# Kernel tuning notes

Measured on AMD Instinct MI355X. Metric: run time of the kernel, lower is better.

The kernel has to match this reference:

```python
import jax, jax.numpy as jnp
import numpy as np

N_NODES = 10000
N_EDGES = 80000
IN_DIM = 768
HID = 256
HEADS = 8
NEG_SLOPE = 0.2


def setup_inputs() -> dict:
    key = jax.random.key(0)
    ks = jax.random.split(key, 12)
    s = 0.02
    x = jax.random.normal(ks[0], (N_NODES, IN_DIM), dtype=jnp.float32)
    edge_index = jax.random.randint(ks[1], (2, N_EDGES), 0, N_NODES, dtype=jnp.int64)
    W1 = jax.random.normal(ks[2], (IN_DIM, HEADS * HID), dtype=jnp.float32) * s
    a_src1 = jax.random.normal(ks[3], (HEADS, HID), dtype=jnp.float32) * s
    a_dst1 = jax.random.normal(ks[4], (HEADS, HID), dtype=jnp.float32) * s
    b1 = jnp.zeros((HEADS * HID,), dtype=jnp.float32)
    W2 = jax.random.normal(ks[5], (HEADS * HID, HEADS * HID), dtype=jnp.float32) * s
    a_src2 = jax.random.normal(ks[6], (HEADS, HID), dtype=jnp.float32) * s
    a_dst2 = jax.random.normal(ks[7], (HEADS, HID), dtype=jnp.float32) * s
    b2 = jnp.zeros((HID,), dtype=jnp.float32)
    # graph_projection: 256 -> 256
    Wp = jax.random.normal(ks[8], (HID, HID), dtype=jnp.float32) * s
    bp = jnp.zeros((HID,), dtype=jnp.float32)
    return dict(x=x, edge_index=edge_index, W1=W1, a_src1=a_src1, a_dst1=a_dst1,
                b1=b1, W2=W2, a_src2=a_src2, a_dst2=a_dst2, b2=b2, Wp=Wp, bp=bp)


def _gat_conv(x, src, dst, W, a_src, a_dst, b, concat):
    """PyG GATConv (eval mode, self-loops already appended to src/dst)."""
    N = x.shape[0]
    H, C = a_src.shape
    h = (x @ W).reshape(N, H, C)                         # [N,H,C] per-head projection
    alpha_s = jnp.sum(h * a_src[None], axis=-1)           # [N,H]
    alpha_d = jnp.sum(h * a_dst[None], axis=-1)           # [N,H]
    e = jax.nn.leaky_relu(alpha_s[src] + alpha_d[dst], NEG_SLOPE)  # [E,H]
    # segment softmax over incoming edges of each dst node
    m = jax.ops.segment_max(e, dst, num_segments=N)       # [N,H]
    m = jnp.where(jnp.isfinite(m), m, 0.0)
    p = jnp.exp(e - m[dst])
    denom = jax.ops.segment_sum(p, dst, num_segments=N)   # [N,H]
    alpha = p / (denom[dst] + 1e-16)                      # [E,H]
    out = jax.ops.segment_sum(alpha[:, :, None] * h[src], dst, num_segments=N)  # [N,H,C]
    if concat:
        return out.reshape(N, H * C) + b
    return out.mean(axis=1) + b


def reference(x, edge_index, W1, a_src1, a_dst1, b1, W2, a_src2, a_dst2, b2, Wp, bp):
    N = x.shape[0]
    loops = jnp.arange(N, dtype=edge_index.dtype)
    src = jnp.concatenate([edge_index[0], loops])
    dst = jnp.concatenate([edge_index[1], loops])
    h = _gat_conv(x, src, dst, W1, a_src1, a_dst1, b1, concat=True)   # [N, 2048]
    h = jax.nn.elu(h)                                                 # dropout: eval/no-op
    h = _gat_conv(h, src, dst, W2, a_src2, a_dst2, b2, concat=False)  # [N, 256]
    h = h @ Wp + bp
    return jax.nn.relu(h)                                             # dropout: eval/no-op
```

## Files before the change

kernel.cpp:

```cpp
#include <hip/hip_runtime.h>
#include <cstdint>
#include <cstddef>

#define IN_DIM  768
#define NNODES  10000
#define MPAD    10240
#define NEDGES  80000
#define E_TOT   90000
#define HEADS   8
#define HID     256
#define HC      2048
#define NEG_SLOPE 0.2f

#define CVT_BLK  ((MPAD * IN_DIM / 4) / 256)
#define CNT_BLK  ((E_TOT + 255) / 256)
#define T1_BLK   ((HC / 32) * (IN_DIM / 32))
#define T2_BLK   ((HC / 32) * (HC / 32))
#define TP_BLK   ((HID / 32) * (HID / 32))
#define PREP_BLK (CVT_BLK + CNT_BLK + T1_BLK + T2_BLK + TP_BLK)

typedef _Float16 __attribute__((ext_vector_type(8))) f16x8;
typedef float    __attribute__((ext_vector_type(4))) f32x4;

__device__ __forceinline__ int edge_src(const int* __restrict__ ei, int e) {
    return (e < NEDGES) ? ei[e] : (e - NEDGES);
}
__device__ __forceinline__ int edge_dst(const int* __restrict__ ei, int e) {
    return (e < NEDGES) ? ei[NEDGES + e] : (e - NEDGES);
}

__device__ __forceinline__ void tcvt_body(
    const float* __restrict__ W, _Float16* __restrict__ T,
    int K, int N, int bx, int by, int t)
{
    __shared__ float tile[32][33];
    int tx = t & 31, ty = t >> 5;
#pragma unroll
    for (int q = 0; q < 4; q++)
        tile[ty + q * 8][tx] = W[(size_t)(by * 32 + ty + q * 8) * N + bx * 32 + tx];
    __syncthreads();
#pragma unroll
    for (int q = 0; q < 4; q++) {
        float v = tile[tx][ty + q * 8];
        T[(size_t)(bx * 32 + ty + q * 8) * K + by * 32 + tx] = (_Float16)v;
    }
}

__global__ __launch_bounds__(256) void prep_kernel(
    const float* __restrict__ x, _Float16* __restrict__ xh,
    const int* __restrict__ ei, int* __restrict__ cnt,
    const float* __restrict__ W1, _Float16* __restrict__ W1t,
    const float* __restrict__ W2, _Float16* __restrict__ W2t,
    const float* __restrict__ Wp, _Float16* __restrict__ Wpt)
{
    int b = blockIdx.x;
    int t = threadIdx.x;
    if (b < CVT_BLK) {
        int i = b * 256 + t;
        size_t e = (size_t)i * 4;
        int r = (int)(e / IN_DIM);
        float4 v = (r < NNODES) ? *(const float4*)(x + e)
                                : make_float4(0.f, 0.f, 0.f, 0.f);
        _Float16 h4[4] = {(_Float16)v.x, (_Float16)v.y, (_Float16)v.z, (_Float16)v.w};
        *(ushort4*)(xh + e) = *(ushort4*)h4;
    } else if (b < CVT_BLK + CNT_BLK) {
        int e = (b - CVT_BLK) * 256 + t;
        if (e < E_TOT) atomicAdd(&cnt[edge_dst(ei, e)], 1);
    } else if (b < CVT_BLK + CNT_BLK + T1_BLK) {
        int idx = b - (CVT_BLK + CNT_BLK);
        tcvt_body(W1, W1t, IN_DIM, HC, idx % (HC / 32), idx / (HC / 32), t);
    } else if (b < CVT_BLK + CNT_BLK + T1_BLK + T2_BLK) {
        int idx = b - (CVT_BLK + CNT_BLK + T1_BLK);
        tcvt_body(W2, W2t, HC, HC, idx % (HC / 32), idx / (HC / 32), t);
    } else {
        int idx = b - (CVT_BLK + CNT_BLK + T1_BLK + T2_BLK);
        tcvt_body(Wp, Wpt, HID, HID, idx % (HID / 32), idx / (HID / 32), t);
    }
}

__global__ void scan_kernel(const int* __restrict__ cnt, int* __restrict__ indptr) {
    __shared__ int sums[1024];
    const int CH = 10;
    int t = threadIdx.x;
    int base = t * CH;
    int s = 0;
#pragma unroll
    for (int i = 0; i < CH; i++) { int idx = base + i; if (idx < NNODES) s += cnt[idx]; }
    sums[t] = s;
    __syncthreads();
    for (int off = 1; off < 1024; off <<= 1) {
        int v = (t >= off) ? sums[t - off] : 0;
        __syncthreads();
        sums[t] += v;
        __syncthreads();
    }
    int run = (t == 0) ? 0 : sums[t - 1];
#pragma unroll
    for (int i = 0; i < CH; i++) {
        int idx = base + i;
        if (idx < NNODES) { indptr[idx] = run; run += cnt[idx]; }
    }
    if (t == 0) indptr[NNODES] = E_TOT;
}

__global__ void scatter_kernel(const int* __restrict__ ei, const int* __restrict__ indptr,
                               int* __restrict__ cur, int* __restrict__ sorted) {
    int e = blockIdx.x * 256 + threadIdx.x;
    if (e < E_TOT) {
        int d = edge_dst(ei, e);
        int pos = atomicAdd(&cur[d], 1);
        sorted[indptr[d] + pos] = e;
    }
}

__global__ __launch_bounds__(512, 2) void gemm8p_kernel(
    const _Float16* __restrict__ A, const _Float16* __restrict__ B,
    _Float16* __restrict__ C, int M, int K, int Nn,
    const float* __restrict__ asrc, const float* __restrict__ adst,
    float* __restrict__ as_out, float* __restrict__ ad_out)
{
    __shared__ __align__(16) _Float16 lds[2][36864];

    const int t = threadIdx.x;
    const int w = t >> 6, lane = t & 63;
    const int fr = lane & 15, q4 = lane >> 4;
    const int wr = w >> 2, wc = w & 3;

    const int nwgx = gridDim.x;
    int wg = blockIdx.y * nwgx + blockIdx.x;
    const int cpx = (nwgx * gridDim.y) >> 3;
    wg = (wg & 7) * cpx + (wg >> 3);
    const int row0 = (wg / nwgx) * 320;
    const int col0 = (wg % nwgx) * 256;

    const int rowt = t >> 3;
    const int scol = ((t & 7) ^ (rowt & 7)) << 3;
    const _Float16* baseA = A + (size_t)(row0 + rowt) * K + scol;
    const _Float16* baseB = B + (size_t)(col0 + rowt) * K + scol;
    const int dstw = w * 512;

    auto stageA = [&](int q, int kel, int bb) {
        __builtin_amdgcn_global_load_lds(
            (const __attribute__((address_space(1))) void*)(baseA + (size_t)q * 64 * K + kel),
            (__attribute__((address_space(3))) void*)&lds[bb][q * 4096 + dstw], 16, 0, 0);
    };
    auto stageB = [&](int q, int kel, int bb) {
        __builtin_amdgcn_global_load_lds(
            (const __attribute__((address_space(1))) void*)(baseB + (size_t)q * 64 * K + kel),
            (__attribute__((address_space(3))) void*)&lds[bb][20480 + q * 4096 + dstw], 16, 0, 0);
    };

    f32x4 acc[2][2][5][2];
#pragma unroll
    for (int qm = 0; qm < 2; qm++)
#pragma unroll
        for (int qn = 0; qn < 2; qn++)
#pragma unroll
            for (int mi = 0; mi < 5; mi++)
#pragma unroll
                for (int ni = 0; ni < 2; ni++)
                    acc[qm][qn][mi][ni] = {0.f, 0.f, 0.f, 0.f};

    f16x8 fa[5][2], fb[2][2][2];

#define LOADA(BB, QM)                                                           \
    {                                                                           \
        _Pragma("unroll")                                                       \
        for (int mi = 0; mi < 5; mi++) {                                        \
            _Pragma("unroll")                                                   \
            for (int ks = 0; ks < 2; ks++) {                                    \
                int lr = wr * 80 + mi * 16 + fr;                                \
                int sl = ((ks << 2) | q4) ^ (fr & 7);                           \
                fa[mi][ks] = *(const f16x8*)&lds[BB][(QM) * 10240 + (lr << 6) + (sl << 3)]; \
            }                                                                   \
        }                                                                       \
    }
#define LOADB(BB, QN)                                                           \
    {                                                                           \
        _Pragma("unroll")                                                       \
        for (int ni = 0; ni < 2; ni++) {                                        \
            _Pragma("unroll")                                                   \
            for (int ks = 0; ks < 2; ks++) {                                    \
                int lr = wc * 32 + ni * 16 + fr;                                \
                int sl = ((ks << 2) | q4) ^ (fr & 7);                           \
                fb[QN][ni][ks] = *(const f16x8*)&lds[BB][20480 + (QN) * 8192 + (lr << 6) + (sl << 3)]; \
            }                                                                   \
        }                                                                       \
    }
#define MFMAQ(QM, QN)                                                           \
    {                                                                           \
        _Pragma("unroll")                                                       \
        for (int ks = 0; ks < 2; ks++) {                                        \
            _Pragma("unroll")                                                   \
            for (int mi = 0; mi < 5; mi++) {                                    \
                _Pragma("unroll")                                               \
                for (int ni = 0; ni < 2; ni++)                                  \
                    acc[QM][QN][mi][ni] = __builtin_amdgcn_mfma_f32_16x16x32_f16(\
                        fa[mi][ks], fb[QN][ni][ks], acc[QM][QN][mi][ni], 0, 0, 0); \
            }                                                                   \
        }                                                                       \
    }
#define LG0 do { asm volatile("s_waitcnt lgkmcnt(0)" ::: "memory");             \
                 __builtin_amdgcn_sched_barrier(0); } while (0)

    stageA(0, 0, 0); stageA(1, 0, 0); stageA(2, 0, 0);
    stageB(0, 0, 0); stageB(1, 0, 0); stageB(2, 0, 0); stageB(3, 0, 0);
    stageA(3, 0, 0); stageA(4, 0, 0);

    const int nT = K >> 6;
    for (int t0 = 0; t0 < nT; ++t0) {
        const int bb = t0 & 1, bn = bb ^ 1, k1 = (t0 + 1) << 6;
        const bool pf = (t0 + 1 < nT);
        asm volatile("s_waitcnt vmcnt(0)" ::: "memory");
        __builtin_amdgcn_s_barrier();

        LOADA(bb, 0); LOADB(bb, 0);
        if (pf) { stageA(0, k1, bn); stageA(1, k1, bn); stageA(2, k1, bn); }
        LG0;
        __builtin_amdgcn_s_setprio(1); MFMAQ(0, 0); __builtin_amdgcn_s_setprio(0);
        __builtin_amdgcn_sched_barrier(0);

        LOADB(bb, 1);
        if (pf) { stageB(0, k1, bn); stageB(1, k1, bn); stageB(2, k1, bn); stageB(3, k1, bn); }
        LG0;
        __builtin_amdgcn_s_setprio(1); MFMAQ(0, 1); __builtin_amdgcn_s_setprio(0);
        __builtin_amdgcn_sched_barrier(0);

        LOADA(bb, 1);
        if (pf) { stageA(3, k1, bn); stageA(4, k1, bn); }
        LG0;
        __builtin_amdgcn_s_setprio(1); MFMAQ(1, 1); MFMAQ(1, 0); __builtin_amdgcn_s_setprio(0);
        __builtin_amdgcn_sched_barrier(0);
    }
#undef LOADA
#undef LOADB
#undef MFMAQ
#undef LG0

#pragma unroll
    for (int qm = 0; qm < 2; qm++)
#pragma unroll
        for (int qn = 0; qn < 2; qn++)
#pragma unroll
            for (int mi = 0; mi < 5; mi++) {
                int mb = row0 + qm * 160 + wr * 80 + mi * 16 + q4 * 4;
#pragma unroll
                for (int ni = 0; ni < 2; ni++) {
                    int n = col0 + qn * 128 + wc * 32 + ni * 16 + fr;
#pragma unroll
                    for (int r = 0; r < 4; r++) {
                        int m = mb + r;
                        if (m < M) C[(size_t)m * Nn + n] = (_Float16)acc[qm][qn][mi][ni][r];
                    }
                }
            }

    if (as_out) {
        __syncthreads();
        float* sAs = (float*)&lds[0][0];
        float* sAd = sAs + 320 * 4;
        float asv[2][2], adv[2][2];
#pragma unroll
        for (int qn = 0; qn < 2; qn++)
#pragma unroll
            for (int ni = 0; ni < 2; ni++) {
                int n = col0 + qn * 128 + wc * 32 + ni * 16 + fr;
                asv[qn][ni] = asrc[n];
                adv[qn][ni] = adst[n];
            }
#pragma unroll
        for (int qm = 0; qm < 2; qm++)
#pragma unroll
            for (int mi = 0; mi < 5; mi++)
#pragma unroll
                for (int r = 0; r < 4; r++) {
                    float sa = 0.f, sd = 0.f;
#pragma unroll
                    for (int qn = 0; qn < 2; qn++)
#pragma unroll
                        for (int ni = 0; ni < 2; ni++) {
                            float v = acc[qm][qn][mi][ni][r];
                            sa = fmaf(v, asv[qn][ni], sa);
                            sd = fmaf(v, adv[qn][ni], sd);
                        }
#pragma unroll
                    for (int o = 1; o < 16; o <<= 1) {
                        sa += __shfl_xor(sa, o, 16);
                        sd += __shfl_xor(sd, o, 16);
                    }
                    if (fr == 0) {
                        int rl = qm * 160 + wr * 80 + mi * 16 + q4 * 4 + r;
                        sAs[rl * 4 + wc] = sa;
                        sAd[rl * 4 + wc] = sd;
                    }
                }
        __syncthreads();
        if (t < 320) {
            float sa = sAs[t * 4] + sAs[t * 4 + 1] + sAs[t * 4 + 2] + sAs[t * 4 + 3];
            float sd = sAd[t * 4] + sAd[t * 4 + 1] + sAd[t * 4 + 2] + sAd[t * 4 + 3];
            int m = row0 + t;
            if (m < M) {
                int head = col0 >> 8;
                as_out[m * HEADS + head] = sa;
                ad_out[m * HEADS + head] = sd;
            }
        }
    }
}

template <int EPI>
__global__ __launch_bounds__(256) void mfma_gemm_kernel(
    const _Float16* __restrict__ A, const _Float16* __restrict__ B,
    void* __restrict__ Cout, const float* __restrict__ bias,
    int M, int K, int Nn, int swz)
{
    __shared__ __align__(16) _Float16 sA[2][128 * 32];
    __shared__ __align__(16) _Float16 sB[2][128 * 32];

    int t = threadIdx.x;
    int bx = blockIdx.x, by = blockIdx.y;
    if (swz) {
        int id = by * 16 + bx;
        int xcd = id & 7, slot = id >> 3;
        bx = 2 * xcd + (slot & 1);
        by = slot >> 1;
    }
    int row0 = by * 128;
    int col0 = bx * 128;

    int s0 = t, s1 = t + 256;
    int m0 = s0 >> 2, k0 = (s0 & 3) * 8;
    int m1 = s1 >> 2, k1 = (s1 & 3) * 8;
    const _Float16* a0 = A + (size_t)(row0 + m0) * K + k0;
    const _Float16* a1 = A + (size_t)(row0 + m1) * K + k1;
    const _Float16* b0 = B + (size_t)(col0 + m0) * K + k0;
    const _Float16* b1 = B + (size_t)(col0 + m1) * K + k1;

    int w = t >> 6, lane = t & 63;
    int wm = (w & 1) * 64, wn = (w >> 1) * 64;
    int fr = lane & 15, quad = lane >> 4;

    auto stage = [&](int kt, int bsel) {
        _Float16* dA0 = &sA[bsel][(w * 64) * 8];
        _Float16* dA1 = &sA[bsel][(w * 64 + 256) * 8];
        _Float16* dB0 = &sB[bsel][(w * 64) * 8];
        _Float16* dB1 = &sB[bsel][(w * 64 + 256) * 8];
        __builtin_amdgcn_global_load_lds(
            (const __attribute__((address_space(1))) void*)(a0 + kt),
            (__attribute__((address_space(3))) void*)dA0, 16, 0, 0);
        __builtin_amdgcn_global_load_lds(
            (const __attribute__((address_space(1))) void*)(a1 + kt),
            (__attribute__((address_space(3))) void*)dA1, 16, 0, 0);
        __builtin_amdgcn_global_load_lds(
            (const __attribute__((address_space(1))) void*)(b0 + kt),
            (__attribute__((address_space(3))) void*)dB0, 16, 0, 0);
        __builtin_amdgcn_global_load_lds(
            (const __attribute__((address_space(1))) void*)(b1 + kt),
            (__attribute__((address_space(3))) void*)dB1, 16, 0, 0);
    };

    f32x4 acc[4][4];
#pragma unroll
    for (int i = 0; i < 4; i++)
#pragma unroll
        for (int j = 0; j < 4; j++) acc[i][j] = {0.f, 0.f, 0.f, 0.f};

    const int nIt = K / 32;
    stage(0, 0);
    __syncthreads();

    for (int it = 0; it < nIt; ++it) {
        int cb = it & 1;
        if (it + 1 < nIt) stage((it + 1) * 32, cb ^ 1);

        f16x8 fa[4], fb[4];
#pragma unroll
        for (int i = 0; i < 4; i++) {
            fa[i] = *(const f16x8*)&sA[cb][(wm + i * 16 + fr) * 32 + quad * 8];
            fb[i] = *(const f16x8*)&sB[cb][(wn + i * 16 + fr) * 32 + quad * 8];
        }
#pragma unroll
        for (int i = 0; i < 4; i++)
#pragma unroll
            for (int j = 0; j < 4; j++)
                acc[i][j] = __builtin_amdgcn_mfma_f32_16x16x32_f16(fa[i], fb[j], acc[i][j], 0, 0, 0);

        if (it + 1 < nIt) __syncthreads();
    }

    if (EPI == 0) {
        _Float16* C = (_Float16*)Cout;
#pragma unroll
        for (int i = 0; i < 4; i++) {
            int mbase = row0 + wm + i * 16 + quad * 4;
#pragma unroll
            for (int j = 0; j < 4; j++) {
                int n = col0 + wn + j * 16 + fr;
#pragma unroll
                for (int r = 0; r < 4; r++) {
                    int m = mbase + r;
                    if (m < M) C[(size_t)m * Nn + n] = (_Float16)acc[i][j][r];
                }
            }
        }
    } else {
        float* C = (float*)Cout;
        float bv[4];
#pragma unroll
        for (int j = 0; j < 4; j++) bv[j] = bias[col0 + wn + j * 16 + fr];
#pragma unroll
        for (int i = 0; i < 4; i++) {
            int mbase = row0 + wm + i * 16 + quad * 4;
#pragma unroll
            for (int j = 0; j < 4; j++) {
                int n = col0 + wn + j * 16 + fr;
#pragma unroll
                for (int r = 0; r < 4; r++) {
                    int m = mbase + r;
                    if (m < M) C[(size_t)m * Nn + n] = fmaxf(acc[i][j][r] + bv[j], 0.f);
                }
            }
        }
    }
}

template <int MODE>
__global__ __launch_bounds__(256) void agg_kernel(
    const _Float16* __restrict__ H, const float* __restrict__ as_,
    const float* __restrict__ ad_, const float* __restrict__ bias,
    const int* __restrict__ indptr, const int* __restrict__ sorted,
    const int* __restrict__ ei, _Float16* __restrict__ outh)
{
    __shared__ float m8[HEADS], d8[HEADS], adl[HEADS];
    __shared__ int   srcl[64];
    __shared__ float al2[HEADS][64];
    __shared__ float red[HC];

    int n = blockIdx.x;
    int t = threadIdx.x;

    if (n >= NNODES) {
        if (MODE == 0) {
            _Float16 z8[8] = {};
            *(f16x8*)&outh[(size_t)n * HC + t * 8] = *(f16x8*)z8;
        } else {
            outh[(size_t)n * HID + t] = (_Float16)0.f;
        }
        return;
    }

    int start = indptr[n];
    int deg = indptr[n + 1] - start;

    if (t < HEADS) adl[t] = ad_[n * HEADS + t];
    __syncthreads();

    int hh = t >> 5, c8 = (t & 31) * 8;
    const size_t hoff = (size_t)hh * HID + c8;
    float acc[8] = {};

    if (deg <= 64) {
        if (t < deg) srcl[t] = edge_src(ei, sorted[start + t]);
        __syncthreads();
        {
            int j = t & 63, h0 = t >> 6;
            if (j < deg) {
                int s = srcl[j];
#pragma unroll
                for (int q = 0; q < 2; q++) {
                    int hx = h0 + q * 4;
                    float v = as_[s * HEADS + hx] + adl[hx];
                    v = (v >= 0.f) ? v : NEG_SLOPE * v;
                    al2[hx][j] = v;
                }
            }
        }
        __syncthreads();
        {
            int h = t >> 5, l = t & 31;
            float mx = -1e30f;
            for (int jj = l; jj < deg; jj += 32) mx = fmaxf(mx, al2[h][jj]);
#pragma unroll
            for (int o = 16; o > 0; o >>= 1) mx = fmaxf(mx, __shfl_xor(mx, o, 32));
            float sm = 0.f;
            for (int jj = l; jj < deg; jj += 32) {
                float e = expf(al2[h][jj] - mx);
                al2[h][jj] = e;
                sm += e;
            }
#pragma unroll
            for (int o = 16; o > 0; o >>= 1) sm += __shfl_xor(sm, o, 32);
            float den = sm + 1e-16f;
            for (int jj = l; jj < deg; jj += 32) al2[h][jj] = al2[h][jj] / den;
        }
        __syncthreads();
        int jj = 0;
        for (; jj + 3 < deg; jj += 4) {
            int sx0 = srcl[jj + 0], sx1 = srcl[jj + 1];
            int sx2 = srcl[jj + 2], sx3 = srcl[jj + 3];
            f16x8 h0v = *(const f16x8*)&H[(size_t)sx0 * HC + hoff];
            f16x8 h1v = *(const f16x8*)&H[(size_t)sx1 * HC + hoff];
            f16x8 h2v = *(const f16x8*)&H[(size_t)sx2 * HC + hoff];
            f16x8 h3v = *(const f16x8*)&H[(size_t)sx3 * HC + hoff];
            float4 a4 = *(const float4*)&al2[hh][jj];
#pragma unroll
            for (int q = 0; q < 8; q++) acc[q] = fmaf(a4.x, (float)h0v[q], acc[q]);
#pragma unroll
            for (int q = 0; q < 8; q++) acc[q] = fmaf(a4.y, (float)h1v[q], acc[q]);
#pragma unroll
            for (int q = 0; q < 8; q++) acc[q] = fmaf(a4.z, (float)h2v[q], acc[q]);
#pragma unroll
            for (int q = 0; q < 8; q++) acc[q] = fmaf(a4.w, (float)h3v[q], acc[q]);
        }
        for (; jj < deg; jj++) {
            int s = srcl[jj];
            f16x8 hv = *(const f16x8*)&H[(size_t)s * HC + hoff];
            float a = al2[hh][jj];
#pragma unroll
            for (int q = 0; q < 8; q++)
                acc[q] = fmaf(a, (float)hv[q], acc[q]);
        }
    } else {
        int h = t >> 5, l = t & 31;
        float adh = adl[h];

        float mx = -1e30f;
        for (int j = l; j < deg; j += 32) {
            int e = sorted[start + j];
            int s = edge_src(ei, e);
            float v = as_[s * HEADS + h] + adh;
            v = (v >= 0.f) ? v : NEG_SLOPE * v;
            mx = fmaxf(mx, v);
        }
#pragma unroll
        for (int o = 16; o > 0; o >>= 1) mx = fmaxf(mx, __shfl_xor(mx, o, 32));

        float sm = 0.f;
        for (int j = l; j < deg; j += 32) {
            int e = sorted[start + j];
            int s = edge_src(ei, e);
            float v = as_[s * HEADS + h] + adh;
            v = (v >= 0.f) ? v : NEG_SLOPE * v;
            sm += expf(v - mx);
        }
#pragma unroll
        for (int o = 16; o > 0; o >>= 1) sm += __shfl_xor(sm, o, 32);
        if (l == 0) { m8[h] = mx; d8[h] = sm; }

        for (int base = 0; base < deg; base += 64) {
            int cntc = min(64, deg - base);
            __syncthreads();
            if (t < cntc) srcl[t] = edge_src(ei, sorted[start + base + t]);
            __syncthreads();
            {
                int j = t & 63, h0 = t >> 6;
                if (j < cntc) {
                    int s = srcl[j];
#pragma unroll
                    for (int q = 0; q < 2; q++) {
                        int hx = h0 + q * 4;
                        float v = as_[s * HEADS + hx] + adl[hx];
                        v = (v >= 0.f) ? v : NEG_SLOPE * v;
                        al2[hx][j] = expf(v - m8[hx]) / (d8[hx] + 1e-16f);
                    }
                }
            }
            __syncthreads();
            int jj = 0;
            for (; jj + 3 < cntc; jj += 4) {
                int sx0 = srcl[jj + 0], sx1 = srcl[jj + 1];
                int sx2 = srcl[jj + 2], sx3 = srcl[jj + 3];
                f16x8 h0v = *(const f16x8*)&H[(size_t)sx0 * HC + hoff];
                f16x8 h1v = *(const f16x8*)&H[(size_t)sx1 * HC + hoff];
                f16x8 h2v = *(const f16x8*)&H[(size_t)sx2 * HC + hoff];
                f16x8 h3v = *(const f16x8*)&H[(size_t)sx3 * HC + hoff];
                float4 a4 = *(const float4*)&al2[hh][jj];
#pragma unroll
                for (int q = 0; q < 8; q++) acc[q] = fmaf(a4.x, (float)h0v[q], acc[q]);
#pragma unroll
                for (int q = 0; q < 8; q++) acc[q] = fmaf(a4.y, (float)h1v[q], acc[q]);
#pragma unroll
                for (int q = 0; q < 8; q++) acc[q] = fmaf(a4.z, (float)h2v[q], acc[q]);
#pragma unroll
                for (int q = 0; q < 8; q++) acc[q] = fmaf(a4.w, (float)h3v[q], acc[q]);
            }
            for (; jj < cntc; jj++) {
                int s = srcl[jj];
                f16x8 hv = *(const f16x8*)&H[(size_t)s * HC + hoff];
                float a = al2[hh][jj];
#pragma unroll
                for (int q = 0; q < 8; q++)
                    acc[q] = fmaf(a, (float)hv[q], acc[q]);
            }
        }
    }

    if (MODE == 0) {
        _Float16 o8[8];
#pragma unroll
        for (int q = 0; q < 8; q++) {
            float v = acc[q] + bias[hoff + q];
            v = (v > 0.f) ? v : expm1f(v);
            o8[q] = (_Float16)v;
        }
        *(f16x8*)&outh[(size_t)n * HC + hoff] = *(f16x8*)o8;
    } else {
#pragma unroll
        for (int q = 0; q < 8; q++) red[hoff + q] = acc[q];
        __syncthreads();
        float s = 0.f;
#pragma unroll
        for (int h2 = 0; h2 < HEADS; h2++) s += red[h2 * HID + t];
        outh[(size_t)n * HID + t] = (_Float16)(s * 0.125f + bias[t]);
    }
}

extern "C" void kernel_launch(void* const* d_in, const int* in_sizes, int n_in,
                              void* d_out, int out_size, void* d_ws, size_t ws_size,
                              hipStream_t stream)
{
    const float* x      = (const float*)d_in[0];
    const int*   ei     = (const int*)  d_in[1];
    const float* W1     = (const float*)d_in[2];
    const float* a_src1 = (const float*)d_in[3];
    const float* a_dst1 = (const float*)d_in[4];
    const float* b1     = (const float*)d_in[5];
    const float* W2     = (const float*)d_in[6];
    const float* a_src2 = (const float*)d_in[7];
    const float* a_dst2 = (const float*)d_in[8];
    const float* b2     = (const float*)d_in[9];
    const float* Wp     = (const float*)d_in[10];
    const float* bp     = (const float*)d_in[11];
    float* out = (float*)d_out;

    char* ws = (char*)d_ws;
    size_t off = 0;
    auto alloc = [&](size_t bytes) -> char* {
        char* p = ws + off;
        off += (bytes + 255) & ~(size_t)255;
        return p;
    };
    _Float16* Hbuf = (_Float16*)alloc((size_t)NNODES * HC * 2);
    _Float16* A2   = (_Float16*)alloc((size_t)MPAD * HC * 2);
    _Float16* W1t  = (_Float16*)alloc((size_t)HC * IN_DIM * 2);
    _Float16* W2t  = (_Float16*)alloc((size_t)HC * HC * 2);
    _Float16* Wpt  = (_Float16*)alloc((size_t)HID * HID * 2);
    _Float16* xh   = (_Float16*)alloc((size_t)MPAD * IN_DIM * 2);
    _Float16* out2h = (_Float16*)alloc((size_t)MPAD * HID * 2);
    float* asad   = (float*)alloc((size_t)4 * NNODES * HEADS * sizeof(float));
    float* as1 = asad;
    float* ad1 = asad + (size_t)NNODES * HEADS;
    float* as2 = asad + (size_t)2 * NNODES * HEADS;
    float* ad2 = asad + (size_t)3 * NNODES * HEADS;
    int*   cntcur = (int*)alloc((size_t)2 * NNODES * sizeof(int));
    int*   cnt = cntcur;
    int*   cur = cntcur + NNODES;
    int*   indptr = (int*)  alloc((size_t)(NNODES + 1) * sizeof(int));
    int*   sorted = (int*)  alloc((size_t)E_TOT * sizeof(int));

    hipMemsetAsync(cntcur, 0, (size_t)2 * NNODES * sizeof(int), stream);
    prep_kernel<<<PREP_BLK, 256, 0, stream>>>(x, xh, ei, cnt,
                                              W1, W1t, W2, W2t, Wp, Wpt);
    scan_kernel<<<1, 1024, 0, stream>>>(cnt, indptr);
    scatter_kernel<<<(E_TOT + 255) / 256, 256, 0, stream>>>(ei, indptr, cur, sorted);

    dim3 g8(HC / 256, MPAD / 320);

    gemm8p_kernel<<<g8, 512, 0, stream>>>(xh, W1t, Hbuf, NNODES, IN_DIM, HC,
                                          a_src1, a_dst1, as1, ad1);
    agg_kernel<0><<<MPAD, 256, 0, stream>>>(Hbuf, as1, ad1, b1, indptr, sorted, ei, A2);

    gemm8p_kernel<<<g8, 512, 0, stream>>>(A2, W2t, Hbuf, NNODES, HC, HC,
                                          a_src2, a_dst2, as2, ad2);
    agg_kernel<1><<<MPAD, 256, 0, stream>>>(Hbuf, as2, ad2, b2, indptr, sorted, ei, out2h);

    dim3 gProj(HID / 128, MPAD / 128);
    mfma_gemm_kernel<1><<<gProj, 256, 0, stream>>>(out2h, Wpt, out, bp,
                                                   NNODES, HID, HID, 0);
}
```

Baseline: 407.8 us.

## Split GEMM main loop into four barrier-gated phases with partial vmcnt waits

The fp16 MFMA GEMM main loop is rebuilt into four phases, each with its own barrier, LDS fragment loads, next-tile global-to-LDS staging and MFMA block. The single `vmcnt(0)` wait at the top of each iteration becomes per-phase partial waits, so a phase only waits for the staged data it needs while later prefetches stay in flight. The last iteration is peeled so the steady-state loop needs no prefetch predicate. This is meant to overlap global loads with MFMA work more finely. It adds more workgroup barriers per tile, and correctness depends on the hard-coded vmcnt counts matching the number of loads each stage call issues.

Result: slower. 422.1 us (+3.5%).

```diff
diff --git a/kernel.cpp b/kernel.cpp
--- a/kernel.cpp
+++ b/kernel.cpp
@@ -187,8 +187,16 @@
             }                                                                   \
         }                                                                       \
     }
-#define MFMAQ(QM, QN)                                                           \
-    {                                                                           \
+
+#define PHASE(QM, QN, LOAD_STMT, STAGE_STMT, WAIT_STMT)                         \
+    do {                                                                        \
+        WAIT_STMT;                                                              \
+        __builtin_amdgcn_s_barrier();                                           \
+        LOAD_STMT;                                                              \
+        STAGE_STMT;                                                             \
+        asm volatile("s_waitcnt lgkmcnt(0)" ::: "memory");                      \
+        __builtin_amdgcn_sched_barrier(0);                                      \
+        __builtin_amdgcn_s_setprio(1);                                          \
         _Pragma("unroll")                                                       \
         for (int ks = 0; ks < 2; ks++) {                                        \
             _Pragma("unroll")                                                   \
@@ -199,43 +207,47 @@
                         fa[mi][ks], fb[QN][ni][ks], acc[QM][QN][mi][ni], 0, 0, 0); \
             }                                                                   \
         }                                                                       \
-    }
-#define LG0 do { asm volatile("s_waitcnt lgkmcnt(0)" ::: "memory");             \
-                 __builtin_amdgcn_sched_barrier(0); } while (0)
+        __builtin_amdgcn_s_setprio(0);                                          \
+        __builtin_amdgcn_sched_barrier(0);                                      \
+    } while (0)
+
+#define VM(N) asm volatile("s_waitcnt vmcnt(" #N ")" ::: "memory")
 
     stageA(0, 0, 0); stageA(1, 0, 0); stageA(2, 0, 0);
-    stageB(0, 0, 0); stageB(1, 0, 0); stageB(2, 0, 0); stageB(3, 0, 0);
+    stageB(0, 0, 0); stageB(1, 0, 0);
+    stageB(2, 0, 0); stageB(3, 0, 0);
     stageA(3, 0, 0); stageA(4, 0, 0);
 
     const int nT = K >> 6;
-    for (int t0 = 0; t0 < nT; ++t0) {
-        const int bb = t0 & 1, bn = bb ^ 1, k1 = (t0 + 1) << 6;
-        const bool pf = (t0 + 1 < nT);
-        asm volatile("s_waitcnt vmcnt(0)" ::: "memory");
-        __builtin_amdgcn_s_barrier();
-
-        LOADA(bb, 0); LOADB(bb, 0);
-        if (pf) { stageA(0, k1, bn); stageA(1, k1, bn); stageA(2, k1, bn); }
-        LG0;
-        __builtin_amdgcn_s_setprio(1); MFMAQ(0, 0); __builtin_amdgcn_s_setprio(0);
-        __builtin_amdgcn_sched_barrier(0);
-
-        LOADB(bb, 1);
-        if (pf) { stageB(0, k1, bn); stageB(1, k1, bn); stageB(2, k1, bn); stageB(3, k1, bn); }
-        LG0;
-        __builtin_amdgcn_s_setprio(1); MFMAQ(0, 1); __builtin_amdgcn_s_setprio(0);
-        __builtin_amdgcn_sched_barrier(0);
-
-        LOADA(bb, 1);
-        if (pf) { stageA(3, k1, bn); stageA(4, k1, bn); }
-        LG0;
-        __builtin_amdgcn_s_setprio(1); MFMAQ(1, 1); MFMAQ(1, 0); __builtin_amdgcn_s_setprio(0);
-        __builtin_amdgcn_sched_barrier(0);
-    }
+    int t0 = 0;
+    for (; t0 < nT - 1; ++t0) {
+        int bb = t0 & 1;
+        int bn = bb ^ 1;
+        int k1 = (t0 + 1) << 6;
+        PHASE(0, 0, { LOADA(bb, 0); LOADB(bb, 0); },
+              { stageA(0, k1, bn); stageA(1, k1, bn); stageA(2, k1, bn); },
+              VM(4));
+        PHASE(0, 1, { LOADB(bb, 1); },
+              { stageB(0, k1, bn); stageB(1, k1, bn); },
+              VM(5));
+        PHASE(1, 1, { LOADA(bb, 1); },
+              { stageB(2, k1, bn); stageB(3, k1, bn); },
+              VM(5));
+        PHASE(1, 0, { },
+              { stageA(3, k1, bn); stageA(4, k1, bn); },
+              ((void)0));
+    }
+    {
+        int bb = t0 & 1;
+        PHASE(0, 0, { LOADA(bb, 0); LOADB(bb, 0); }, ((void)0), VM(4));
+        PHASE(0, 1, { LOADB(bb, 1); },               ((void)0), VM(2));
+        PHASE(1, 1, { LOADA(bb, 1); },               ((void)0), VM(0));
+        PHASE(1, 0, { },                             ((void)0), ((void)0));
+    }
+#undef PHASE
 #undef LOADA
 #undef LOADB
-#undef MFMAQ
-#undef LG0
+#undef VM
 
 #pragma unroll
     for (int qm = 0; qm < 2; qm++)
```
